# Optimization experiments

Hardware: AMD Instinct MI355X
Metric: run time of the kernel (lower is better)

## Reference

```python
import jax, jax.numpy as jnp
import numpy as np

B, N, D = 512, 100000, 256
MAX_K = 20
EPS = 1e-12


def setup_inputs() -> dict:
    key = jax.random.key(0)
    k1, k2, k3, k4 = jax.random.split(key, 4)
    z_ego = jax.random.normal(k1, (B, D), dtype=jnp.float32)
    exo_bank = jax.random.normal(k2, (N, D), dtype=jnp.float32)
    sim_vt = jax.random.uniform(k3, (B, N), dtype=jnp.float32)
    W = jax.random.normal(k4, (D, D), dtype=jnp.float32) / np.sqrt(D)
    return {"z_ego": z_ego, "exo_bank": exo_bank, "sim_vt": sim_vt, "W": W, "k": 16}


def _l2_normalize(x):
    # matches torch F.normalize semantics with eps clamp
    n = jnp.sqrt(jnp.sum(x * x, axis=-1, keepdims=True))
    return x / jnp.maximum(n, EPS)


def reference(z_ego, exo_bank, sim_vt, W, k):
    # bilinear projection into query space (Linear, no bias)
    q = z_ego @ W.T                              # [B, D]
    k_eff = min(int(k), MAX_K, exo_bank.shape[0])
    # pairwise cosine similarity query x bank
    sim_vv = _l2_normalize(q) @ _l2_normalize(exo_bank).T   # [B, N]
    # combined score (sim_vt already [B, N]; broadcast is identity)
    score = 0.5 * sim_vv + 0.5 * sim_vt          # [B, N]
    _, topk_idx = jax.lax.top_k(score, k_eff)    # [B, k_eff]
    gathered = exo_bank[topk_idx]                # [B, k_eff, D]
    return gathered, topk_idx
```

## Files before the change

kernel.cpp:

```cpp
#include <hip/hip_runtime.h>
#include <math.h>
#include <stdint.h>

#define B_Q    512
#define N_BANK 100000
#define D_DIM  256
#define K16    16

#define NSL2   256
#define NCHUNK 1563
#define TROW   264
#define CHUNK_USHORT (64 * TROW)
#define CHUNK_BYTES  (CHUNK_USHORT * 2)
#define NGRP   6250
#define GSTRIDE 6272
#define MARGIN 5e-3f
#define CAPG   384

#define OFF_QN     0
#define OFF_QNT    0x80000
#define OFF_INORM  0x100000
#define OFF_TH     0x170000
#define OFF_GMAX   0x400000
#define OFF_BANKT  0x1400000
#define WS_NEED    ((size_t)OFF_BANKT + (size_t)NCHUNK * CHUNK_BYTES)

#define FB_OFF_INORM (B_Q * D_DIM * 4)
#define FB_OFF_PSC   (1024 * 1024)
#define FB_OFF_PID   (FB_OFF_PSC + B_Q * 128 * K16 * 4)

typedef __attribute__((ext_vector_type(8))) short short8;
typedef __attribute__((ext_vector_type(4))) float floatx4;

typedef __attribute__((address_space(1))) const unsigned char gu8_t;
typedef __attribute__((address_space(3))) unsigned char lu8_t;

__device__ inline unsigned short f2bf(float x) {
    unsigned int u = __float_as_uint(x);
    unsigned int r = (u + 0x7FFFu + ((u >> 16) & 1u)) >> 16;
    return (unsigned short)r;
}
__device__ inline unsigned long long pack_key(float s, int idx) {
    unsigned int u = __float_as_uint(s);
    u ^= (u & 0x80000000u) ? 0xFFFFFFFFu : 0x80000000u;
    return ((unsigned long long)u << 32) | (unsigned int)(~(unsigned int)idx);
}
__device__ inline int key_idx(unsigned long long k) {
    return (int)(~(unsigned int)(k & 0xFFFFFFFFull));
}
__device__ inline unsigned long long shfl_down_u64(unsigned long long x, int off) {
    unsigned int lo = (unsigned int)x;
    unsigned int hi = (unsigned int)(x >> 32);
    lo = __shfl_down(lo, off, 64);
    hi = __shfl_down(hi, off, 64);
    return ((unsigned long long)hi << 32) | lo;
}
__device__ inline unsigned long long umax64(unsigned long long a, unsigned long long b) {
    return a > b ? a : b;
}


__global__ void qn_prep_kernel(const float* __restrict__ z_ego,
                               const float* __restrict__ W,
                               float* __restrict__ qn,
                               unsigned short* __restrict__ qnt) {
    __shared__ float zs[D_DIM];
    __shared__ float red[4];
    int b = blockIdx.x;
    int t = threadIdx.x;
    zs[t] = z_ego[b * D_DIM + t];
    __syncthreads();
    const float4* W4 = reinterpret_cast<const float4*>(W + (size_t)t * D_DIM);
    float acc = 0.f;
#pragma unroll 8
    for (int u = 0; u < 64; ++u) {
        float4 w = W4[u];
        acc += w.x * zs[u * 4 + 0];
        acc += w.y * zs[u * 4 + 1];
        acc += w.z * zs[u * 4 + 2];
        acc += w.w * zs[u * 4 + 3];
    }
    float ss = acc * acc;
#pragma unroll
    for (int off = 32; off > 0; off >>= 1) ss += __shfl_down(ss, off, 64);
    if ((t & 63) == 0) red[t >> 6] = ss;
    __syncthreads();
    float tot = red[0] + red[1] + red[2] + red[3];
    float n = fmaxf(sqrtf(tot), 1e-12f);
    float v = acc / n;
    qn[b * D_DIM + t] = v;
    qnt[(size_t)(b >> 6) * CHUNK_USHORT + (size_t)(b & 63) * TROW + t] = f2bf(v);
}

__global__ __launch_bounds__(256)
void prep_bank_kernel(const float* __restrict__ bank,
                      float* __restrict__ inorm,
                      unsigned short* __restrict__ bankt) {
    int c = blockIdx.x;
    int t = threadIdx.x, w = t >> 6, l = t & 63;
    unsigned short* dst = bankt + (size_t)c * CHUNK_USHORT;
#pragma unroll 1
    for (int rr = 0; rr < 16; ++rr) {
        int row = w * 16 + rr;
        int jg = c * 64 + row;
        ushort4 o = {0, 0, 0, 0};
        if (jg < N_BANK) {
            float4 v = *reinterpret_cast<const float4*>(bank + (size_t)jg * D_DIM + l * 4);
            float ss = v.x * v.x + v.y * v.y + v.z * v.z + v.w * v.w;
#pragma unroll
            for (int off = 1; off < 64; off <<= 1) ss += __shfl_xor(ss, off, 64);
            float inv = 1.0f / fmaxf(sqrtf(ss), 1e-12f);
            o.x = f2bf(v.x * inv); o.y = f2bf(v.y * inv);
            o.z = f2bf(v.z * inv); o.w = f2bf(v.w * inv);
            if (l == 0) inorm[jg] = inv;
        }
        *reinterpret_cast<ushort4*>(dst + (size_t)row * TROW + l * 4) = o;
    }
}

__global__ __launch_bounds__(256, 4)
void screen4_kernel(const unsigned short* __restrict__ qnt,
                    const unsigned short* __restrict__ bankt,
                    const float* __restrict__ svt,
                    float* __restrict__ gmax) {
    __shared__ unsigned short lbank[CHUNK_USHORT];
    int t = threadIdx.x, w = t >> 6, l = t & 63;
    int lane16 = l & 15, quad = l >> 4;

    int bid = blockIdx.x;
    int xcd = bid & 7;
    int i = bid >> 3;
    int slice = (xcd << 5) + (i >> 2);
    int qb = i & 3;

    int qt = qb * 4 + w;
    int qbase = qt * 32;

    short8 afrag[2][8];
    {
        const unsigned short* abase = qnt + (size_t)(qt >> 1) * CHUNK_USHORT
                                          + (size_t)((qt & 1) * 32) * TROW;
#pragma unroll
        for (int s = 0; s < 2; ++s)
#pragma unroll
            for (int k = 0; k < 8; ++k)
                afrag[s][k] = *reinterpret_cast<const short8*>(
                    abase + (size_t)(16 * s + lane16) * TROW + k * 32 + quad * 8);
    }

    const float* svr[2][4];
#pragma unroll
    for (int s = 0; s < 2; ++s)
#pragma unroll
        for (int r = 0; r < 4; ++r)
            svr[s][r] = svt + (size_t)(qbase + 16 * s + 4 * quad + r) * (size_t)N_BANK;

    for (int c = slice; c < NCHUNK; c += NSL2) {
        int j0 = c * 64;

        {
            const unsigned char* gsrc = (const unsigned char*)bankt + (size_t)c * CHUNK_BYTES;
            unsigned char* lbase = (unsigned char*)lbank;
#pragma unroll
            for (int i2 = 0; i2 < 8; ++i2) {
                int off = i2 * 4096 + w * 1024;
                __builtin_amdgcn_global_load_lds((gu8_t*)(gsrc + off + l * 16),
                                                 (lu8_t*)(lbase + off), 16, 0, 0);
            }
            int off8 = 32768 + w * 256;
            __builtin_amdgcn_global_load_lds((gu8_t*)(gsrc + off8 + l * 4),
                                             (lu8_t*)(lbase + off8), 4, 0, 0);
        }

        float sv[4][2][4];
#pragma unroll
        for (int s = 0; s < 2; ++s)
#pragma unroll
            for (int r = 0; r < 4; ++r) {
                const float* rp = svr[s][r] + j0 + lane16;
#pragma unroll
                for (int jg = 0; jg < 4; ++jg) {
                    int jglob = j0 + 16 * jg + lane16;
                    sv[jg][s][r] = (jglob < N_BANK) ? rp[16 * jg] : 0.f;
                }
            }

        __syncthreads();

        int g0 = c * 4;
#pragma unroll
        for (int jg = 0; jg < 4; ++jg) {
            floatx4 acc0 = (floatx4){0.f, 0.f, 0.f, 0.f};
            floatx4 acc1 = (floatx4){0.f, 0.f, 0.f, 0.f};
            const unsigned short* bbase = lbank + (size_t)(16 * jg + lane16) * TROW + quad * 8;
#pragma unroll
            for (int k = 0; k < 8; ++k) {
                short8 bfrag = *reinterpret_cast<const short8*>(bbase + k * 32);
                acc0 = __builtin_amdgcn_mfma_f32_16x16x32_bf16(afrag[0][k], bfrag, acc0, 0, 0, 0);
                acc1 = __builtin_amdgcn_mfma_f32_16x16x32_bf16(afrag[1][k], bfrag, acc1, 0, 0, 0);
            }

            int jglob = j0 + 16 * jg + lane16;
            bool inb = jglob < N_BANK;
            int g = g0 + jg;
            bool doStore = (lane16 == 0) && (g < NGRP);
#pragma unroll
            for (int s = 0; s < 2; ++s) {
#pragma unroll
                for (int r = 0; r < 4; ++r) {
                    float a = (s == 0) ? acc0[r] : acc1[r];
                    float score = inb ? (0.5f * a + 0.5f * sv[jg][s][r]) : -INFINITY;
                    score = fmaxf(score, __shfl_xor(score, 1, 64));
                    score = fmaxf(score, __shfl_xor(score, 2, 64));
                    score = fmaxf(score, __shfl_xor(score, 4, 64));
                    score = fmaxf(score, __shfl_xor(score, 8, 64));
                    if (doStore) {
                        int q = qbase + 16 * s + 4 * quad + r;
                        gmax[(size_t)q * GSTRIDE + g] = score;
                    }
                }
            }
        }
        __syncthreads();
    }
}

__global__ __launch_bounds__(256)
void gthresh_kernel(const float* __restrict__ gmax,
                    float* __restrict__ th) {
    __shared__ float buf[NGRP];
    __shared__ float red[4];
    int q = blockIdx.x, t = threadIdx.x, w = t >> 6;
    for (int i = t; i < NGRP; i += 256) buf[i] = gmax[(size_t)q * GSTRIDE + i];
    __syncthreads();
    float s16 = -INFINITY;
    for (int r = 0; r < K16; ++r) {
        float m = -INFINITY;
        for (int i = t; i < NGRP; i += 256) m = fmaxf(m, buf[i]);
#pragma unroll
        for (int off = 32; off > 0; off >>= 1) m = fmaxf(m, __shfl_down(m, off, 64));
        if ((t & 63) == 0) red[w] = m;
        __syncthreads();
        m = fmaxf(fmaxf(red[0], red[1]), fmaxf(red[2], red[3]));
        if (r == K16 - 1) s16 = m;
        if (r < K16 - 1) {
            for (int i = t; i < NGRP; i += 256)
                if (buf[i] == m) buf[i] = -INFINITY;
        }
        __syncthreads();
    }
    if (t == 0) th[q] = s16 - MARGIN;
}

__global__ __launch_bounds__(256)
void grescore_kernel(const float* __restrict__ gmax,
                     const float* __restrict__ th,
                     const float* __restrict__ qn,
                     const float* __restrict__ inorm,
                     const float* __restrict__ bank,
                     const float* __restrict__ svt,
                     float* __restrict__ out) {
    __shared__ float qns[D_DIM];
    __shared__ int glist[CAPG];
    __shared__ unsigned long long keys2[CAPG * K16];
    __shared__ unsigned long long wred[4];
    __shared__ int winI[K16];
    __shared__ int gcntS;
    int b = blockIdx.x, t = threadIdx.x;
    int w = t >> 6, l = t & 63;

    qns[t] = qn[(size_t)b * D_DIM + t];
    if (t == 0) gcntS = 0;
    __syncthreads();
    float thb = th[b];
    for (int g = t; g < NGRP; g += 256) {
        if (gmax[(size_t)b * GSTRIDE + g] >= thb) {
            int p = atomicAdd(&gcntS, 1);
            if (p < CAPG) glist[p] = g;
        }
    }
    __syncthreads();
    int ng = gcntS < CAPG ? gcntS : CAPG;
    int ncand = ng * K16;

    const float4* bank4 = reinterpret_cast<const float4*>(bank);
    float4 qv = reinterpret_cast<const float4*>(qns)[l];
    for (int ci = w; ci < ncand; ci += 8) {
        int jA = glist[ci >> 4] * K16 + (ci & 15);
        int ci2 = ci + 4;
        bool has2 = ci2 < ncand;
        int jB = has2 ? (glist[ci2 >> 4] * K16 + (ci2 & 15)) : jA;
        float4 bvA = bank4[(size_t)jA * 64 + l];
        float4 bvB = bank4[(size_t)jB * 64 + l];
        float dA = qv.x * bvA.x + qv.y * bvA.y + qv.z * bvA.z + qv.w * bvA.w;
        float dB = qv.x * bvB.x + qv.y * bvB.y + qv.z * bvB.z + qv.w * bvB.w;
#pragma unroll
        for (int off = 32; off > 0; off >>= 1) dA += __shfl_down(dA, off, 64);
#pragma unroll
        for (int off = 32; off > 0; off >>= 1) dB += __shfl_down(dB, off, 64);
        if (l == 0) {
            float sA = 0.5f * (dA * inorm[jA]) + 0.5f * svt[(size_t)b * N_BANK + jA];
            keys2[ci] = pack_key(sA, jA);
            if (has2) {
                float sB = 0.5f * (dB * inorm[jB]) + 0.5f * svt[(size_t)b * N_BANK + jB];
                keys2[ci2] = pack_key(sB, jB);
            }
        }
    }
    __syncthreads();

    for (int r = 0; r < K16; ++r) {
        unsigned long long best = 0ull;
        for (int i2 = t; i2 < ncand; i2 += 256) best = umax64(best, keys2[i2]);
#pragma unroll
        for (int off = 32; off > 0; off >>= 1) best = umax64(best, shfl_down_u64(best, off));
        if (l == 0) wred[w] = best;
        __syncthreads();
        unsigned long long W = umax64(umax64(wred[0], wred[1]), umax64(wred[2], wred[3]));
        if (t == 0) winI[r] = key_idx(W);
        for (int i2 = t; i2 < ncand; i2 += 256)
            if (keys2[i2] == W) keys2[i2] = 0ull;
        __syncthreads();
    }

    if (t < K16)
        out[(size_t)B_Q * K16 * D_DIM + (size_t)b * K16 + t] = (float)winI[t];
    float4* out4 = reinterpret_cast<float4*>(out);
    for (int u = t; u < K16 * 64; u += 256) {
        int r = u >> 6, cc = u & 63;
        out4[((size_t)b * K16 + r) * 64 + cc] = bank4[(size_t)winI[r] * 64 + cc];
    }
}

#define FBT 64
#define FJT 64
#define FKC 64
#define FNS 128
#define FNC ((N_BANK + FJT - 1) / FJT)

__global__ void inorm_kernel(const float* __restrict__ bank,
                             float* __restrict__ inorm) {
    int w = threadIdx.x >> 6;
    int lane = threadIdx.x & 63;
    int j = blockIdx.x * 4 + w;
    if (j >= N_BANK) return;
    const float4* r4 = reinterpret_cast<const float4*>(bank + (size_t)j * D_DIM);
    float4 v = r4[lane];
    float ss = v.x * v.x + v.y * v.y + v.z * v.z + v.w * v.w;
#pragma unroll
    for (int off = 32; off > 0; off >>= 1) ss += __shfl_down(ss, off, 64);
    if (lane == 0) inorm[j] = 1.0f / fmaxf(sqrtf(ss), 1e-12f);
}

__global__ void fb_qn_kernel(const float* __restrict__ z_ego,
                             const float* __restrict__ W,
                             float* __restrict__ qn) {
    __shared__ float zs[D_DIM];
    __shared__ float red[4];
    int b = blockIdx.x;
    int t = threadIdx.x;
    zs[t] = z_ego[b * D_DIM + t];
    __syncthreads();
    const float4* W4 = reinterpret_cast<const float4*>(W + (size_t)t * D_DIM);
    float acc = 0.f;
#pragma unroll 8
    for (int u = 0; u < 64; ++u) {
        float4 w = W4[u];
        acc += w.x * zs[u * 4 + 0]; acc += w.y * zs[u * 4 + 1];
        acc += w.z * zs[u * 4 + 2]; acc += w.w * zs[u * 4 + 3];
    }
    float ss = acc * acc;
#pragma unroll
    for (int off = 32; off > 0; off >>= 1) ss += __shfl_down(ss, off, 64);
    if ((t & 63) == 0) red[t >> 6] = ss;
    __syncthreads();
    float tot = red[0] + red[1] + red[2] + red[3];
    qn[b * D_DIM + t] = acc / fmaxf(sqrtf(tot), 1e-12f);
}

__global__ __launch_bounds__(256)
void fb_score_topk_kernel(const float* __restrict__ qn,
                          const float* __restrict__ bank,
                          const float* __restrict__ svt,
                          const float* __restrict__ inorm,
                          float* __restrict__ psc,
                          int* __restrict__ pid) {
    __shared__ float As[FKC][FBT];
    __shared__ float Bsh[FKC][FJT];
    __shared__ float Ss[FBT][FJT + 1];
    int slice = blockIdx.x;
    int qbase = blockIdx.y * FBT;
    int t = threadIdx.x;
    int tq = t >> 4, tj = t & 15;
    int q0 = tq * 4, j0l = tj * 4;
    float sc[K16]; int id[K16];
#pragma unroll
    for (int i = 0; i < K16; ++i) { sc[i] = -INFINITY; id[i] = 0x7fffffff; }
    for (int c = slice; c < FNC; c += FNS) {
        int j0 = c * FJT;
        float acc[4][4];
#pragma unroll
        for (int a = 0; a < 4; ++a)
#pragma unroll
            for (int b2 = 0; b2 < 4; ++b2) acc[a][b2] = 0.f;
        for (int kc = 0; kc < D_DIM; kc += FKC) {
            __syncthreads();
#pragma unroll
            for (int r = 0; r < 4; ++r) {
                int idx = t + 256 * r;
                int q = idx & 63, kv = idx >> 6;
                float4 v = *reinterpret_cast<const float4*>(
                    &qn[(size_t)(qbase + q) * D_DIM + kc + kv * 4]);
                As[kv * 4 + 0][q] = v.x; As[kv * 4 + 1][q] = v.y;
                As[kv * 4 + 2][q] = v.z; As[kv * 4 + 3][q] = v.w;
            }
#pragma unroll
            for (int r = 0; r < 4; ++r) {
                int idx = t + 256 * r;
                int j = idx & 63, kv = idx >> 6;
                int jg = j0 + j;
                float4 v = make_float4(0.f, 0.f, 0.f, 0.f);
                if (jg < N_BANK)
                    v = *reinterpret_cast<const float4*>(
                        &bank[(size_t)jg * D_DIM + kc + kv * 4]);
                Bsh[kv * 4 + 0][j] = v.x; Bsh[kv * 4 + 1][j] = v.y;
                Bsh[kv * 4 + 2][j] = v.z; Bsh[kv * 4 + 3][j] = v.w;
            }
            __syncthreads();
#pragma unroll
            for (int k = 0; k < FKC; ++k) {
                float4 av = *reinterpret_cast<const float4*>(&As[k][q0]);
                float4 bv = *reinterpret_cast<const float4*>(&Bsh[k][j0l]);
                float a[4] = {av.x, av.y, av.z, av.w};
                float bb[4] = {bv.x, bv.y, bv.z, bv.w};
#pragma unroll
                for (int qi = 0; qi < 4; ++qi)
#pragma unroll
                    for (int ji = 0; ji < 4; ++ji) acc[qi][ji] += a[qi] * bb[ji];
            }
        }
        bool full = (j0 + FJT <= N_BANK);
        if (full) {
            float4 inv = *reinterpret_cast<const float4*>(&inorm[j0 + j0l]);
            float iv[4] = {inv.x, inv.y, inv.z, inv.w};
#pragma unroll
            for (int qi = 0; qi < 4; ++qi) {
                int q = qbase + q0 + qi;
                float4 svv = *reinterpret_cast<const float4*>(
                    &svt[(size_t)q * N_BANK + j0 + j0l]);
                float s[4] = {svv.x, svv.y, svv.z, svv.w};
#pragma unroll
                for (int ji = 0; ji < 4; ++ji)
                    Ss[q0 + qi][j0l + ji] = 0.5f * (acc[qi][ji] * iv[ji]) + 0.5f * s[ji];
            }
        } else {
#pragma unroll
            for (int qi = 0; qi < 4; ++qi) {
                int q = qbase + q0 + qi;
#pragma unroll
                for (int ji = 0; ji < 4; ++ji) {
                    int jg = j0 + j0l + ji;
                    float s = -INFINITY;
                    if (jg < N_BANK)
                        s = 0.5f * (acc[qi][ji] * inorm[jg]) + 0.5f * svt[(size_t)q * N_BANK + jg];
                    Ss[q0 + qi][j0l + ji] = s;
                }
            }
        }
        __syncthreads();
        if (t < FBT) {
#pragma unroll 1
            for (int jj = 0; jj < FJT; ++jj) {
                int jg = j0 + jj;
                if (jg >= N_BANK) break;
                float s = Ss[t][jj];
                if (s > sc[K16 - 1] || (s == sc[K16 - 1] && jg < id[K16 - 1])) {
                    float cs = s; int ci = jg;
#pragma unroll
                    for (int i = 0; i < K16; ++i) {
                        bool bt2 = (cs > sc[i]) || (cs == sc[i] && ci < id[i]);
                        float ts = sc[i]; int ti = id[i];
                        if (bt2) { sc[i] = cs; id[i] = ci; cs = ts; ci = ti; }
                    }
                }
            }
        }
    }
    if (t < FBT) {
        int q = qbase + t;
        size_t base = ((size_t)q * FNS + slice) * K16;
#pragma unroll
        for (int i = 0; i < K16; ++i) { psc[base + i] = sc[i]; pid[base + i] = id[i]; }
    }
}

__global__ __launch_bounds__(256)
void fb_merge_kernel(const float* __restrict__ psc,
                     const int* __restrict__ pid,
                     const float* __restrict__ bank,
                     float* __restrict__ out) {
    __shared__ unsigned long long keys[FNS * K16];
    __shared__ unsigned long long wred[4];
    __shared__ int win[K16];
    int b = blockIdx.x, t = threadIdx.x;
    for (int i = t; i < FNS * K16; i += 256) {
        float s = psc[(size_t)b * FNS * K16 + i];
        unsigned int u = __float_as_uint(s);
        u ^= (u & 0x80000000u) ? 0xFFFFFFFFu : 0x80000000u;
        unsigned int iv = ~(unsigned int)pid[(size_t)b * FNS * K16 + i];
        keys[i] = ((unsigned long long)u << 32) | iv;
    }
    __syncthreads();
    for (int r = 0; r < K16; ++r) {
        unsigned long long best = 0ull;
        for (int i = t; i < FNS * K16; i += 256) best = umax64(best, keys[i]);
#pragma unroll
        for (int off = 32; off > 0; off >>= 1) best = umax64(best, shfl_down_u64(best, off));
        if ((t & 63) == 0) wred[t >> 6] = best;
        __syncthreads();
        unsigned long long w = umax64(umax64(wred[0], wred[1]), umax64(wred[2], wred[3]));
        if (t == 0) win[r] = (int)(~(unsigned int)w);
        for (int i = t; i < FNS * K16; i += 256)
            if (keys[i] == w) keys[i] = 0ull;
        __syncthreads();
    }
    if (t < K16)
        out[(size_t)B_Q * K16 * D_DIM + (size_t)b * K16 + t] = (float)win[t];
    const float4* bank4 = reinterpret_cast<const float4*>(bank);
    float4* out4 = reinterpret_cast<float4*>(out);
    for (int u = t; u < K16 * 64; u += 256) {
        int r = u >> 6, c = u & 63;
        out4[((size_t)b * K16 + r) * 64 + c] = bank4[(size_t)win[r] * 64 + c];
    }
}

extern "C" void kernel_launch(void* const* d_in, const int* in_sizes, int n_in,
                              void* d_out, int out_size, void* d_ws, size_t ws_size,
                              hipStream_t stream) {
    const float* z_ego = (const float*)d_in[0];
    const float* bank  = (const float*)d_in[1];
    const float* svt   = (const float*)d_in[2];
    const float* W     = (const float*)d_in[3];
    float* out = (float*)d_out;
    char* ws = (char*)d_ws;

    if (ws_size >= WS_NEED) {
        float* qn             = (float*)(ws + OFF_QN);
        unsigned short* qnt   = (unsigned short*)(ws + OFF_QNT);
        float* inorm          = (float*)(ws + OFF_INORM);
        float* th             = (float*)(ws + OFF_TH);
        float* gmax           = (float*)(ws + OFF_GMAX);
        unsigned short* bankt = (unsigned short*)(ws + OFF_BANKT);

        qn_prep_kernel<<<B_Q, 256, 0, stream>>>(z_ego, W, qn, qnt);
        prep_bank_kernel<<<NCHUNK, 256, 0, stream>>>(bank, inorm, bankt);
        screen4_kernel<<<NSL2 * 4, 256, 0, stream>>>(qnt, bankt, svt, gmax);
        gthresh_kernel<<<B_Q, 256, 0, stream>>>(gmax, th);
        grescore_kernel<<<B_Q, 256, 0, stream>>>(gmax, th, qn, inorm, bank, svt, out);
    } else {
        float* qn    = (float*)(ws + 0);
        float* inorm = (float*)(ws + FB_OFF_INORM);
        float* psc   = (float*)(ws + FB_OFF_PSC);
        int*   pid   = (int*)(ws + FB_OFF_PID);
        fb_qn_kernel<<<B_Q, 256, 0, stream>>>(z_ego, W, qn);
        inorm_kernel<<<(N_BANK + 3) / 4, 256, 0, stream>>>(bank, inorm);
        dim3 grid(FNS, B_Q / FBT);
        fb_score_topk_kernel<<<grid, 256, 0, stream>>>(qn, bank, svt, inorm, psc, pid);
        fb_merge_kernel<<<B_Q, 256, 0, stream>>>(psc, pid, bank, out);
    }
}
```

Measured before the change: 698.7 us.

## Repack sim_vt into per-chunk slabs before screening for contiguous loads

Adds a transpose/repack kernel that copies sim_vt into chunk-major slabs (64 columns by 512 queries per chunk), and a screen5 kernel that reads those slabs instead of striding across 100000-wide rows. The aim is to make each chunk's sim_vt reads contiguous and cache-friendly inside the screening kernel. In exchange the whole 200MB sim_vt is read and written one extra time, which is substantial extra memory traffic. The new path only runs if the workspace is large enough.

```diff
diff --git a/kernel.cpp b/kernel.cpp
--- a/kernel.cpp
+++ b/kernel.cpp
@@ -17,6 +17,8 @@
 #define MARGIN 5e-3f
 #define CAPG   384
 
+#define SLAB_FLOATS 32768
+
 #define OFF_QN     0
 #define OFF_QNT    0x80000
 #define OFF_INORM  0x100000
@@ -24,6 +26,8 @@
 #define OFF_GMAX   0x400000
 #define OFF_BANKT  0x1400000
 #define WS_NEED    ((size_t)OFF_BANKT + (size_t)NCHUNK * CHUNK_BYTES)
+#define OFF_SVTT   0x4800000
+#define WS_NEED2   ((size_t)OFF_SVTT + (size_t)NCHUNK * SLAB_FLOATS * 4)
 
 #define FB_OFF_INORM (B_Q * D_DIM * 4)
 #define FB_OFF_PSC   (1024 * 1024)
@@ -118,6 +122,148 @@
     }
 }
 
+#define RT_Q 8
+#define RT_J 1024
+__global__ __launch_bounds__(256)
+void svt_repack_kernel(const float* __restrict__ svt,
+                       float* __restrict__ svtt) {
+    __shared__ float tile[RT_Q][RT_J + 4];
+    int t = threadIdx.x;
+    int jt = blockIdx.x;
+    int q0 = blockIdx.y * RT_Q;
+    int jl = t * 4;
+#pragma unroll
+    for (int qq = 0; qq < RT_Q; ++qq) {
+        int j = jt * RT_J + jl;
+        float4 v = make_float4(0.f, 0.f, 0.f, 0.f);
+        if (j < N_BANK)
+            v = *reinterpret_cast<const float4*>(svt + (size_t)(q0 + qq) * N_BANK + j);
+        *reinterpret_cast<float4*>(&tile[qq][jl]) = v;
+    }
+    __syncthreads();
+    int half = t >> 7;
+    int q1 = (t >> 4) & 7;
+    int m = t & 15;
+#pragma unroll
+    for (int p = 0; p < 8; ++p) {
+        int cc = p * 2 + half;
+        int c = jt * 16 + cc;
+        if (c < NCHUNK) {
+            float4 v = *reinterpret_cast<const float4*>(&tile[q1][cc * 64 + m * 4]);
+            *reinterpret_cast<float4*>(svtt + (size_t)c * SLAB_FLOATS
+                                       + (size_t)(q0 + q1) * 64 + m * 4) = v;
+        }
+    }
+}
+
+__global__ __launch_bounds__(256, 4)
+void screen5_kernel(const unsigned short* __restrict__ qnt,
+                    const unsigned short* __restrict__ bankt,
+                    const float* __restrict__ svtt,
+                    float* __restrict__ gmax) {
+    __shared__ unsigned short lbank[CHUNK_USHORT];
+    int t = threadIdx.x, w = t >> 6, l = t & 63;
+    int lane16 = l & 15, quad = l >> 4;
+
+    int bid = blockIdx.x;
+    int xcd = bid & 7;
+    int i = bid >> 3;
+    int slice = (xcd << 5) + (i >> 2);
+    int qb = i & 3;
+
+    int qt = qb * 4 + w;
+    int qbase = qt * 32;
+
+    short8 afrag[2][8];
+    {
+        const unsigned short* abase = qnt + (size_t)(qt >> 1) * CHUNK_USHORT
+                                          + (size_t)((qt & 1) * 32) * TROW;
+#pragma unroll
+        for (int s = 0; s < 2; ++s)
+#pragma unroll
+            for (int k = 0; k < 8; ++k)
+                afrag[s][k] = *reinterpret_cast<const short8*>(
+                    abase + (size_t)(16 * s + lane16) * TROW + k * 32 + quad * 8);
+    }
+
+    const float* sp[2][4];
+#pragma unroll
+    for (int s = 0; s < 2; ++s)
+#pragma unroll
+        for (int r = 0; r < 4; ++r)
+            sp[s][r] = svtt + (size_t)(qbase + 16 * s + 4 * quad + r) * 64 + lane16;
+
+    for (int c = slice; c < NCHUNK; c += NSL2) {
+        int j0 = c * 64;
+
+        {
+            const unsigned char* gsrc = (const unsigned char*)bankt + (size_t)c * CHUNK_BYTES;
+            unsigned char* lbase = (unsigned char*)lbank;
+#pragma unroll
+            for (int i2 = 0; i2 < 8; ++i2) {
+                int off = i2 * 4096 + w * 1024;
+                __builtin_amdgcn_global_load_lds((gu8_t*)(gsrc + off + l * 16),
+                                                 (lu8_t*)(lbase + off), 16, 0, 0);
+            }
+            int off8 = 32768 + w * 256;
+            __builtin_amdgcn_global_load_lds((gu8_t*)(gsrc + off8 + l * 4),
+                                             (lu8_t*)(lbase + off8), 4, 0, 0);
+        }
+
+        float sv[4][2][4];
+        {
+            size_t slabOff = (size_t)c * SLAB_FLOATS;
+#pragma unroll
+            for (int s = 0; s < 2; ++s)
+#pragma unroll
+                for (int r = 0; r < 4; ++r) {
+                    const float* rp = sp[s][r] + slabOff;
+#pragma unroll
+                    for (int jg = 0; jg < 4; ++jg)
+                        sv[jg][s][r] = rp[16 * jg];
+                }
+        }
+
+        __syncthreads();
+
+        int g0 = c * 4;
+#pragma unroll
+        for (int jg = 0; jg < 4; ++jg) {
+            floatx4 acc0 = (floatx4){0.f, 0.f, 0.f, 0.f};
+            floatx4 acc1 = (floatx4){0.f, 0.f, 0.f, 0.f};
+            const unsigned short* bbase = lbank + (size_t)(16 * jg + lane16) * TROW + quad * 8;
+#pragma unroll
+            for (int k = 0; k < 8; ++k) {
+                short8 bfrag = *reinterpret_cast<const short8*>(bbase + k * 32);
+                acc0 = __builtin_amdgcn_mfma_f32_16x16x32_bf16(afrag[0][k], bfrag, acc0, 0, 0, 0);
+                acc1 = __builtin_amdgcn_mfma_f32_16x16x32_bf16(afrag[1][k], bfrag, acc1, 0, 0, 0);
+            }
+
+            int jglob = j0 + 16 * jg + lane16;
+            bool inb = jglob < N_BANK;
+            int g = g0 + jg;
+            bool doStore = (lane16 == 0) && (g < NGRP);
+#pragma unroll
+            for (int s = 0; s < 2; ++s) {
+#pragma unroll
+                for (int r = 0; r < 4; ++r) {
+                    float a = (s == 0) ? acc0[r] : acc1[r];
+                    float score = inb ? (0.5f * a + 0.5f * sv[jg][s][r]) : -INFINITY;
+                    score = fmaxf(score, __shfl_xor(score, 1, 64));
+                    score = fmaxf(score, __shfl_xor(score, 2, 64));
+                    score = fmaxf(score, __shfl_xor(score, 4, 64));
+                    score = fmaxf(score, __shfl_xor(score, 8, 64));
+                    if (doStore) {
+                        int q = qbase + 16 * s + 4 * quad + r;
+                        gmax[(size_t)q * GSTRIDE + g] = score;
+                    }
+                }
+            }
+        }
+        __syncthreads();
+    }
+}
+
 __global__ __launch_bounds__(256, 4)
 void screen4_kernel(const unsigned short* __restrict__ qnt,
                     const unsigned short* __restrict__ bankt,
@@ -157,7 +303,6 @@
 
     for (int c = slice; c < NCHUNK; c += NSL2) {
         int j0 = c * 64;
-
         {
             const unsigned char* gsrc = (const unsigned char*)bankt + (size_t)c * CHUNK_BYTES;
             unsigned char* lbase = (unsigned char*)lbank;
@@ -554,7 +699,14 @@
 
         qn_prep_kernel<<<B_Q, 256, 0, stream>>>(z_ego, W, qn, qnt);
         prep_bank_kernel<<<NCHUNK, 256, 0, stream>>>(bank, inorm, bankt);
-        screen4_kernel<<<NSL2 * 4, 256, 0, stream>>>(qnt, bankt, svt, gmax);
+        if (ws_size >= WS_NEED2) {
+            float* svtt = (float*)(ws + OFF_SVTT);
+            dim3 rg((N_BANK + RT_J - 1) / RT_J, B_Q / RT_Q);
+            svt_repack_kernel<<<rg, 256, 0, stream>>>(svt, svtt);
+            screen5_kernel<<<NSL2 * 4, 256, 0, stream>>>(qnt, bankt, svtt, gmax);
+        } else {
+            screen4_kernel<<<NSL2 * 4, 256, 0, stream>>>(qnt, bankt, svt, gmax);
+        }
         gthresh_kernel<<<B_Q, 256, 0, stream>>>(gmax, th);
         grescore_kernel<<<B_Q, 256, 0, stream>>>(gmax, th, qn, inorm, bank, svt, out);
     } else {
```

New measurement: 677.5 us. 3.0% less time.
